# Optimization experiments

Hardware: AMD Instinct MI355X
Metric: run time of the kernel (lower is better)

The kernel has to match this reference:

```python
import jax, jax.numpy as jnp
import numpy as np
from jax import lax

B, S, F, C = 64, 2048, 256, 32


def setup_inputs() -> dict:
    key = jax.random.key(0)
    ks = jax.random.split(key, 6)
    return {
        "X": jax.random.normal(ks[0], (B, S, F), dtype=jnp.float32),
        "W": jax.random.normal(ks[1], (C, F), dtype=jnp.float32) * (1.0 / np.sqrt(F)),
        "b": jax.random.normal(ks[2], (C,), dtype=jnp.float32) * 0.01,
        "transitions": jax.random.normal(ks[3], (C, C), dtype=jnp.float32) * 0.1,
        "start_transitions": jax.random.normal(ks[4], (C,), dtype=jnp.float32) * 0.1,
        "end_transitions": jax.random.normal(ks[5], (C,), dtype=jnp.float32) * 0.1,
    }


def reference(X, W, b, transitions, start_transitions, end_transitions):
    # Affine projection to emission scores: [B, S, C]
    emissions = jnp.einsum("bsf,cf->bsc", X, W) + b
    e = jnp.moveaxis(emissions, 1, 0)  # [S, B, C] for scan over time

    alpha0 = start_transitions[None, :] + e[0]  # [B, C]

    def viterbi_step(alpha, e_t):
        # scores[b, i, j] = alpha[b, i] + T[i, j] + e_t[b, j]
        scores = alpha[:, :, None] + transitions[None, :, :] + e_t[:, None, :]
        best = jnp.max(scores, axis=1)      # [B, C]
        bp = jnp.argmax(scores, axis=1)     # [B, C] backpointers
        return best, bp

    alpha_T, backptrs = lax.scan(viterbi_step, alpha0, e[1:])  # backptrs: [S-1, B, C]

    final = alpha_T + end_transitions[None, :]
    best_score = jnp.max(final, axis=-1)              # [B]
    last_tag = jnp.argmax(final, axis=-1)             # [B]

    def backtrack(tag, bp):
        prev = jnp.take_along_axis(bp, tag[:, None], axis=1)[:, 0]
        return prev, prev

    _, prev_tags = lax.scan(backtrack, last_tag, backptrs, reverse=True)  # [S-1, B]
    path = jnp.concatenate([prev_tags, last_tag[None, :]], axis=0)        # [S, B]
    return best_score, jnp.moveaxis(path, 0, 1)  # ([B], [B, S])
```

## Files before the change

kernel.cpp:

```cpp
#include <hip/hip_runtime.h>

#define BB 64
#define SS 2048
#define FF 256
#define CC 32

typedef unsigned u32x2 __attribute__((ext_vector_type(2)));

__device__ __forceinline__ void plswap16(int a_in, int& x, int& y) {
#if __has_builtin(__builtin_amdgcn_permlane16_swap)
    u32x2 r = __builtin_amdgcn_permlane16_swap((unsigned)a_in, (unsigned)a_in, false, false);
    x = (int)r[0]; y = (int)r[1];
#else
    int xx = a_in, yy;
    asm volatile("v_mov_b32 %0, %1" : "=v"(yy) : "v"(a_in));
    asm volatile("v_permlane16_swap_b32 %0, %1" : "+v"(xx), "+v"(yy));
    x = xx; y = yy;
#endif
}
__device__ __forceinline__ void plswap32(int a_in, int& x, int& y) {
#if __has_builtin(__builtin_amdgcn_permlane32_swap)
    u32x2 r = __builtin_amdgcn_permlane32_swap((unsigned)a_in, (unsigned)a_in, false, false);
    x = (int)r[0]; y = (int)r[1];
#else
    int xx = a_in, yy;
    asm volatile("v_mov_b32 %0, %1" : "=v"(yy) : "v"(a_in));
    asm volatile("v_permlane32_swap_b32 %0, %1" : "+v"(xx), "+v"(yy));
    x = xx; y = yy;
#endif
}

#if __has_builtin(__builtin_amdgcn_mov_dpp)
#define ROT1(d, s, K) d = __builtin_amdgcn_mov_dpp(s, 0x120 + K, 0xF, 0xF, false)
#else
#define ROT1(d, s, K) d = __builtin_amdgcn_update_dpp(s, s, 0x120 + K, 0xF, 0xF, false)
#endif
#define ROTALL(arr, s) \
    arr[0] = s;        \
    ROT1(arr[1], s, 1);  ROT1(arr[2], s, 2);  ROT1(arr[3], s, 3);  \
    ROT1(arr[4], s, 4);  ROT1(arr[5], s, 5);  ROT1(arr[6], s, 6);  \
    ROT1(arr[7], s, 7);  ROT1(arr[8], s, 8);  ROT1(arr[9], s, 9);  \
    ROT1(arr[10], s, 10); ROT1(arr[11], s, 11); ROT1(arr[12], s, 12); \
    ROT1(arr[13], s, 13); ROT1(arr[14], s, 14); ROT1(arr[15], s, 15)

__device__ __forceinline__ float fmax3_(float a, float b, float c) { return fmaxf(fmaxf(a, b), c); }

__global__ __launch_bounds__(256) void emis_kernel(const float* __restrict__ X,
                                                   const float* __restrict__ W,
                                                   const float* __restrict__ bias,
                                                   float* __restrict__ em) {
    __shared__ __align__(16) float xs[64 * 260];
    __shared__ __align__(16) float wsh[32 * 260];
    const int tid = threadIdx.x;
    const long rowbase = (long)blockIdx.x * 64;

    const float4* Xg = (const float4*)(X + rowbase * FF);
#pragma unroll
    for (int i = 0; i < 16; ++i) {
        int idx = tid + i * 256;
        int r = idx >> 6, c4 = idx & 63;
        *(float4*)&xs[r * 260 + c4 * 4] = Xg[idx];
    }
    const float4* Wg = (const float4*)W;
#pragma unroll
    for (int i = 0; i < 8; ++i) {
        int idx = tid + i * 256;
        int r = idx >> 6, c4 = idx & 63;
        *(float4*)&wsh[r * 260 + c4 * 4] = Wg[idx];
    }
    __syncthreads();

    const int rp = tid >> 3;
    const int cg = (tid & 7) * 4;
    const int r0 = rp * 2, r1 = rp * 2 + 1;
    float acc0[4] = {0.f, 0.f, 0.f, 0.f};
    float acc1[4] = {0.f, 0.f, 0.f, 0.f};

#pragma unroll 4
    for (int k = 0; k < 256; k += 4) {
        float4 xa = *(const float4*)&xs[r0 * 260 + k];
        float4 xb = *(const float4*)&xs[r1 * 260 + k];
#pragma unroll
        for (int jj = 0; jj < 4; ++jj) {
            float4 w = *(const float4*)&wsh[(cg + jj) * 260 + k];
            acc0[jj] = fmaf(xa.x, w.x, acc0[jj]);
            acc0[jj] = fmaf(xa.y, w.y, acc0[jj]);
            acc0[jj] = fmaf(xa.z, w.z, acc0[jj]);
            acc0[jj] = fmaf(xa.w, w.w, acc0[jj]);
            acc1[jj] = fmaf(xb.x, w.x, acc1[jj]);
            acc1[jj] = fmaf(xb.y, w.y, acc1[jj]);
            acc1[jj] = fmaf(xb.z, w.z, acc1[jj]);
            acc1[jj] = fmaf(xb.w, w.w, acc1[jj]);
        }
    }
#pragma unroll
    for (int jj = 0; jj < 4; ++jj) {
        float bj = bias[cg + jj];
        em[(rowbase + r0) * CC + cg + jj] = acc0[jj] + bj;
        em[(rowbase + r1) * CC + cg + jj] = acc1[jj] + bj;
    }
}

#define STEP_ASM(avar, evar)                                                        \
    do {                                                                            \
        float x_, y_, b_, q0_, q1_, q2_, q3_, q4_, q5_, q6_, q7_,                   \
              q8_, q9_, q10_, q11_, q12_, q13_, q14_, q15_;                         \
        asm volatile(                                                               \
            "v_mov_b32 %[x], %[aa]\n\t"                                             \
            "s_nop 1\n\t"                                                           \
            "v_permlane16_swap_b32 %[x], %[aa]\n\t"                                 \
            "s_nop 0\n\t"                                                           \
            "v_cndmask_b32 %[bb], %[aa], %[x], %[m16]\n\t"                          \
            "s_nop 1\n\t"                                                           \
            "v_add_f32 %[q0], %[bb], %[t0]\n\t"                                     \
            "v_add_f32_dpp %[q1], %[bb], %[t1] row_ror:1 row_mask:0xf bank_mask:0xf\n\t"  \
            "v_add_f32_dpp %[q2], %[bb], %[t2] row_ror:2 row_mask:0xf bank_mask:0xf\n\t"  \
            "v_add_f32_dpp %[q3], %[bb], %[t3] row_ror:3 row_mask:0xf bank_mask:0xf\n\t"  \
            "v_add_f32_dpp %[q4], %[bb], %[t4] row_ror:4 row_mask:0xf bank_mask:0xf\n\t"  \
            "v_add_f32_dpp %[q5], %[bb], %[t5] row_ror:5 row_mask:0xf bank_mask:0xf\n\t"  \
            "v_add_f32_dpp %[q6], %[bb], %[t6] row_ror:6 row_mask:0xf bank_mask:0xf\n\t"  \
            "v_add_f32_dpp %[q7], %[bb], %[t7] row_ror:7 row_mask:0xf bank_mask:0xf\n\t"  \
            "v_add_f32_dpp %[q8], %[bb], %[t8] row_ror:8 row_mask:0xf bank_mask:0xf\n\t"  \
            "v_add_f32_dpp %[q9], %[bb], %[t9] row_ror:9 row_mask:0xf bank_mask:0xf\n\t"  \
            "v_add_f32_dpp %[q10], %[bb], %[t10] row_ror:10 row_mask:0xf bank_mask:0xf\n\t" \
            "v_add_f32_dpp %[q11], %[bb], %[t11] row_ror:11 row_mask:0xf bank_mask:0xf\n\t" \
            "v_add_f32_dpp %[q12], %[bb], %[t12] row_ror:12 row_mask:0xf bank_mask:0xf\n\t" \
            "v_add_f32_dpp %[q13], %[bb], %[t13] row_ror:13 row_mask:0xf bank_mask:0xf\n\t" \
            "v_add_f32_dpp %[q14], %[bb], %[t14] row_ror:14 row_mask:0xf bank_mask:0xf\n\t" \
            "v_add_f32_dpp %[q15], %[bb], %[t15] row_ror:15 row_mask:0xf bank_mask:0xf\n\t" \
            "v_max3_f32 %[q0], %[q0], %[q1], %[q2]\n\t"                             \
            "v_max3_f32 %[q3], %[q3], %[q4], %[q5]\n\t"                             \
            "v_max3_f32 %[q6], %[q6], %[q7], %[q8]\n\t"                             \
            "v_max3_f32 %[q9], %[q9], %[q10], %[q11]\n\t"                           \
            "v_max3_f32 %[q12], %[q12], %[q13], %[q14]\n\t"                         \
            "v_max3_f32 %[q0], %[q0], %[q3], %[q6]\n\t"                             \
            "v_max3_f32 %[q9], %[q9], %[q12], %[q15]\n\t"                           \
            "v_max_f32 %[q0], %[q0], %[q9]\n\t"                                     \
            "v_mov_b32 %[x], %[q0]\n\t"                                             \
            "v_mov_b32 %[y], %[q0]\n\t"                                             \
            "s_nop 1\n\t"                                                           \
            "v_permlane32_swap_b32 %[x], %[y]\n\t"                                  \
            "s_nop 0\n\t"                                                           \
            "v_cndmask_b32 %[y], %[y], %[x], %[m32]\n\t"                            \
            "v_max_f32 %[q0], %[q0], %[y]\n\t"                                      \
            "v_add_f32 %[aa], %[q0], %[ee]\n\t"                                     \
            : [aa] "+v"(avar), [x] "=&v"(x_), [y] "=&v"(y_), [bb] "=&v"(b_),        \
              [q0] "=&v"(q0_), [q1] "=&v"(q1_), [q2] "=&v"(q2_), [q3] "=&v"(q3_),   \
              [q4] "=&v"(q4_), [q5] "=&v"(q5_), [q6] "=&v"(q6_), [q7] "=&v"(q7_),   \
              [q8] "=&v"(q8_), [q9] "=&v"(q9_), [q10] "=&v"(q10_),                  \
              [q11] "=&v"(q11_), [q12] "=&v"(q12_), [q13] "=&v"(q13_),              \
              [q14] "=&v"(q14_), [q15] "=&v"(q15_)                                  \
            : [ee] "v"(evar), [t0] "v"(Ti[0]), [t1] "v"(Ti[1]), [t2] "v"(Ti[2]),    \
              [t3] "v"(Ti[3]), [t4] "v"(Ti[4]), [t5] "v"(Ti[5]), [t6] "v"(Ti[6]),   \
              [t7] "v"(Ti[7]), [t8] "v"(Ti[8]), [t9] "v"(Ti[9]), [t10] "v"(Ti[10]), \
              [t11] "v"(Ti[11]), [t12] "v"(Ti[12]), [t13] "v"(Ti[13]),              \
              [t14] "v"(Ti[14]), [t15] "v"(Ti[15]),                                 \
              [m16] "s"(mask16), [m32] "s"(mask32));                                \
    } while (0)

__global__ __launch_bounds__(64, 1) void viterbi_fwd4(float* __restrict__ em,
                                                      const float* __restrict__ T,
                                                      const float* __restrict__ startT,
                                                      const float* __restrict__ endT,
                                                      float* __restrict__ out) {
    const int l = threadIdx.x;
    const int b = blockIdx.x;
    const int j = l & 31;
    const int h = l >> 5;

    int p0, p1;
    plswap16(j, p0, p1);
    const bool c16 = (((p0 >> 4) & 1) == h);
    const int pm = c16 ? p0 : p1;
    int mk[16];
    ROTALL(mk, pm);
    int q0, q1;
    plswap32(l, q0, q1);
    const bool pick0 = (q0 == (l ^ 32));

    const unsigned long long mask16 = __ballot(c16);
    const unsigned long long mask32 = __ballot(pick0);

    float Ti[16];
#pragma unroll
    for (int k = 0; k < 16; ++k) Ti[k] = T[mk[k] * CC + j];

    float* eb = em + (long)b * SS * CC;

    float eq[8];
#pragma unroll
    for (int v = 0; v < 8; ++v) eq[v] = eb[v * 32 + j];

    float a = startT[j] + eq[0];
    eb[j] = a;
    eq[0] = eb[8 * 32 + j];

    int t = 1;
    for (int g = 0; g < 254; ++g) {
#pragma unroll
        for (int u = 0; u < 8; ++u) {
            STEP_ASM(a, eq[t & 7]);
            eb[t * 32 + j] = a;
            eq[t & 7] = eb[(t + 8) * 32 + j];
            ++t;
        }
    }
#pragma unroll
    for (int u = 0; u < 7; ++u) {
        STEP_ASM(a, eq[t & 7]);
        eb[t * 32 + j] = a;
        eq[t & 7] = eb[(t + 8) * 32 + j];
        ++t;
    }
#pragma unroll
    for (int u = 0; u < 8; ++u) {
        STEP_ASM(a, eq[t & 7]);
        eb[t * 32 + j] = a;
        ++t;
    }

    float v = a + endT[j];
    int idx = j;
#pragma unroll
    for (int d = 1; d <= 16; d <<= 1) {
        float ovv = __shfl_xor(v, d);
        int   oii = __shfl_xor(idx, d);
        bool c = (ovv > v) || (ovv == v && oii < idx);
        v = c ? ovv : v;
        idx = c ? oii : idx;
    }
    if (l == 0) {
        out[b] = v;
        out[BB + (long)b * SS + (SS - 1)] = (float)idx;
    }
}

__global__ __launch_bounds__(64, 2) void bp_compose(const float* __restrict__ alpha,
                                                    const float* __restrict__ T,
                                                    unsigned* __restrict__ bp,
                                                    unsigned char* __restrict__ G) {
    const int l = threadIdx.x;
    const int j = l & 31;
    const int h = l >> 5;
    const int b = blockIdx.x >> 5;
    const int k = blockIdx.x & 31;

    int p0, p1;
    plswap16(j, p0, p1);
    const bool c16 = (((p0 >> 4) & 1) == h);
    const int pm = c16 ? p0 : p1;
    int mk[16];
    ROTALL(mk, pm);
    int q0, q1;
    plswap32(l, q0, q1);
    const bool pick0 = (q0 == (l ^ 32));

    float Ti[16];
    unsigned Bk[16];
#pragma unroll
    for (int kk = 0; kk < 16; ++kk) {
        Ti[kk] = T[mk[kk] * CC + j];
        Bk[kk] = 1u << mk[kk];
    }

    const float* A = alpha + (long)b * SS * CC;
    const int kk0 = k << 6;

    float aq[8];
#pragma unroll
    for (int v = 0; v < 8; ++v) aq[v] = A[(kk0 + v) * CC + j];

    unsigned sr[16];
#pragma unroll
    for (int p = 0; p < 16; ++p) sr[p] = 0u;

#pragma unroll
    for (int g8 = 0; g8 < 8; ++g8) {
#pragma unroll
        for (int v = 0; v < 8; ++v) {
            const int u = g8 * 8 + v;
            float av = aq[v];
            if (g8 < 7) aq[v] = A[(kk0 + (g8 + 1) * 8 + v) * CC + j];

            int x, y;
            plswap16(__float_as_int(av), x, y);
            int base = c16 ? x : y;
            int rot[16];
            ROTALL(rot, base);
            float s[16];
#pragma unroll
            for (int kk = 0; kk < 16; ++kk) s[kk] = __int_as_float(rot[kk]) + Ti[kk];

            float m0 = fmax3_(s[0], s[1], s[2]);
            float m1 = fmax3_(s[3], s[4], s[5]);
            float m2 = fmax3_(s[6], s[7], s[8]);
            float m3 = fmax3_(s[9], s[10], s[11]);
            float m4 = fmax3_(s[12], s[13], s[14]);
            float mv = fmaxf(fmax3_(m0, m1, m2), fmax3_(m3, m4, s[15]));

            int xm, ym;
            plswap32(__float_as_int(mv), xm, ym);
            float ov = __int_as_float(pick0 ? xm : ym);
            float gv = fmaxf(mv, ov);

            unsigned c0 = (s[0] == gv) ? Bk[0] : 0u,   c1 = (s[1] == gv) ? Bk[1] : 0u;
            unsigned c2 = (s[2] == gv) ? Bk[2] : 0u,   c3 = (s[3] == gv) ? Bk[3] : 0u;
            unsigned c4 = (s[4] == gv) ? Bk[4] : 0u,   c5 = (s[5] == gv) ? Bk[5] : 0u;
            unsigned c6 = (s[6] == gv) ? Bk[6] : 0u,   c7 = (s[7] == gv) ? Bk[7] : 0u;
            unsigned c8 = (s[8] == gv) ? Bk[8] : 0u,   c9 = (s[9] == gv) ? Bk[9] : 0u;
            unsigned c10 = (s[10] == gv) ? Bk[10] : 0u, c11 = (s[11] == gv) ? Bk[11] : 0u;
            unsigned c12 = (s[12] == gv) ? Bk[12] : 0u, c13 = (s[13] == gv) ? Bk[13] : 0u;
            unsigned c14 = (s[14] == gv) ? Bk[14] : 0u, c15 = (s[15] == gv) ? Bk[15] : 0u;
            unsigned msk = ((c0 | c1 | c2) | (c3 | c4 | c5)) |
                           ((c6 | c7 | c8) | (c9 | c10 | c11)) |
                           ((c12 | c13 | c14) | c15);

            int xk, yk;
            plswap32((int)msk, xk, yk);
            unsigned om = (unsigned)(pick0 ? xk : yk);
            int wi = __builtin_ctz(msk | om);

            if (u == 63) {
                if (kk0 + 63 == SS - 1) wi = j;
            }
            sr[u >> 2] |= (unsigned)wi << ((u & 3) * 8);
        }
    }

#pragma unroll
    for (int p = 0; p < 16; ++p)
        bp[((unsigned)(16 * k + p) * BB + b) * CC + j] = sr[p];

    int g = j;
#pragma unroll
    for (int rel = 63; rel >= 0; --rel) {
        unsigned dw = (unsigned)__builtin_amdgcn_ds_bpermute((g | (l & 32)) << 2,
                                                             (int)sr[rel >> 2]);
        g = (int)((dw >> ((rel & 3) * 8)) & 31u);
    }
    G[(b * 32 + k) * 32 + j] = (unsigned char)g;
}

__global__ __launch_bounds__(64) void bt_emit2(const unsigned* __restrict__ bp,
                                               const unsigned char* __restrict__ G,
                                               float* __restrict__ out) {
    const int l = threadIdx.x;
    const int b = blockIdx.x >> 5;
    const int k = blockIdx.x & 31;

    unsigned sr[16];
#pragma unroll
    for (int p = 0; p < 16; ++p) sr[p] = bp[((unsigned)(16 * k + p) * BB + b) * CC + (l & 31)];

    int cur = (int)out[BB + (long)b * SS + (SS - 1)];
    for (int kk = 31; kk > k; --kk) cur = (int)G[(b * 32 + kk) * 32 + cur];

    int g = cur, cap = cur;
#pragma unroll
    for (int rel = 63; rel >= 0; --rel) {
        unsigned dw = (unsigned)__builtin_amdgcn_ds_bpermute((g | (l & 32)) << 2,
                                                             (int)sr[rel >> 2]);
        g = (int)((dw >> ((rel & 3) * 8)) & 31u);
        cap = (l == rel) ? g : cap;
    }
    out[BB + (long)b * SS + k * 64 + l] = (float)cap;
}

extern "C" void kernel_launch(void* const* d_in, const int* in_sizes, int n_in,
                              void* d_out, int out_size, void* d_ws, size_t ws_size,
                              hipStream_t stream) {
    const float* X      = (const float*)d_in[0];
    const float* W      = (const float*)d_in[1];
    const float* bias   = (const float*)d_in[2];
    const float* T      = (const float*)d_in[3];
    const float* startT = (const float*)d_in[4];
    const float* endT   = (const float*)d_in[5];
    float* out = (float*)d_out;

    float*    em = (float*)d_ws;
    unsigned* bp = (unsigned*)((char*)d_ws + (size_t)BB * SS * CC * 4);
    unsigned char* G = (unsigned char*)d_ws + (20u << 20);

    emis_kernel<<<(BB * SS) / 64, 256, 0, stream>>>(X, W, bias, em);
    viterbi_fwd4<<<BB, 64, 0, stream>>>(em, T, startT, endT, out);
    bp_compose<<<BB * 32, 64, 0, stream>>>(em, T, bp, G);
    bt_emit2<<<BB * 32, 64, 0, stream>>>(bp, G, out);
}
```

Baseline: 307.9 us.

## Fuse forward recursion with backpointer compose via LDS ring and flag sync

The forward max-plus recursion now runs on one wave per batch row and writes alpha into an 8-slot shared-memory ring. Three helper waves in the same block poll a progress flag and compute backpointers and 64-step chunk compositions concurrently, so the separate bp_compose kernel and the global alpha round trip go away. The suffix composition over chunks moves into a single-block bt_scan kernel, replacing the per-block quadratic G walk in the emit kernel. The step also drops a mask-select after the permlane32 swap. The risks are a ring-overrun race if the consumer waves fall behind, spin-wait overhead, and only one block per batch row.

Measured after the change: 323.8 us. 1.05x slower.

```diff
diff --git a/kernel.cpp b/kernel.cpp
--- a/kernel.cpp
+++ b/kernel.cpp
@@ -101,9 +101,9 @@
     }
 }
 
-#define STEP_ASM(avar, evar)                                                        \
+#define STEP2_ASM(avar, evar)                                                       \
     do {                                                                            \
-        float x_, y_, b_, q0_, q1_, q2_, q3_, q4_, q5_, q6_, q7_,                   \
+        float x_, b_, q0_, q1_, q2_, q3_, q4_, q5_, q6_, q7_,                       \
               q8_, q9_, q10_, q11_, q12_, q13_, q14_, q15_;                         \
         asm volatile(                                                               \
             "v_mov_b32 %[x], %[aa]\n\t"                                             \
@@ -137,14 +137,12 @@
             "v_max3_f32 %[q9], %[q9], %[q12], %[q15]\n\t"                           \
             "v_max_f32 %[q0], %[q0], %[q9]\n\t"                                     \
             "v_mov_b32 %[x], %[q0]\n\t"                                             \
-            "v_mov_b32 %[y], %[q0]\n\t"                                             \
             "s_nop 1\n\t"                                                           \
-            "v_permlane32_swap_b32 %[x], %[y]\n\t"                                  \
+            "v_permlane32_swap_b32 %[x], %[q0]\n\t"                                 \
             "s_nop 0\n\t"                                                           \
-            "v_cndmask_b32 %[y], %[y], %[x], %[m32]\n\t"                            \
-            "v_max_f32 %[q0], %[q0], %[y]\n\t"                                      \
+            "v_max_f32 %[q0], %[q0], %[x]\n\t"                                      \
             "v_add_f32 %[aa], %[q0], %[ee]\n\t"                                     \
-            : [aa] "+v"(avar), [x] "=&v"(x_), [y] "=&v"(y_), [bb] "=&v"(b_),        \
+            : [aa] "+v"(avar), [x] "=&v"(x_), [bb] "=&v"(b_),                       \
               [q0] "=&v"(q0_), [q1] "=&v"(q1_), [q2] "=&v"(q2_), [q3] "=&v"(q3_),   \
               [q4] "=&v"(q4_), [q5] "=&v"(q5_), [q6] "=&v"(q6_), [q7] "=&v"(q7_),   \
               [q8] "=&v"(q8_), [q9] "=&v"(q9_), [q10] "=&v"(q10_),                  \
@@ -155,18 +153,28 @@
               [t7] "v"(Ti[7]), [t8] "v"(Ti[8]), [t9] "v"(Ti[9]), [t10] "v"(Ti[10]), \
               [t11] "v"(Ti[11]), [t12] "v"(Ti[12]), [t13] "v"(Ti[13]),              \
               [t14] "v"(Ti[14]), [t15] "v"(Ti[15]),                                 \
-              [m16] "s"(mask16), [m32] "s"(mask32));                                \
+              [m16] "s"(mask16));                                                   \
     } while (0)
 
-__global__ __launch_bounds__(64, 1) void viterbi_fwd4(float* __restrict__ em,
-                                                      const float* __restrict__ T,
-                                                      const float* __restrict__ startT,
-                                                      const float* __restrict__ endT,
-                                                      float* __restrict__ out) {
-    const int l = threadIdx.x;
+__global__ __launch_bounds__(256, 1) void viterbi_fused(const float* __restrict__ em,
+                                                        const float* __restrict__ T,
+                                                        const float* __restrict__ startT,
+                                                        const float* __restrict__ endT,
+                                                        unsigned* __restrict__ bp,
+                                                        unsigned char* __restrict__ G,
+                                                        float* __restrict__ out) {
+    __shared__ float aring[8 * 2048];
+    __shared__ int prog;
+
+    const int tid = threadIdx.x;
+    const int w = tid >> 6;
+    const int l = tid & 63;
     const int b = blockIdx.x;
     const int j = l & 31;
     const int h = l >> 5;
+
+    if (tid == 0) prog = 0;
+    __syncthreads();
 
     int p0, p1;
     plswap16(j, p0, p1);
@@ -174,176 +182,204 @@
     const int pm = c16 ? p0 : p1;
     int mk[16];
     ROTALL(mk, pm);
-    int q0, q1;
-    plswap32(l, q0, q1);
-    const bool pick0 = (q0 == (l ^ 32));
-
-    const unsigned long long mask16 = __ballot(c16);
-    const unsigned long long mask32 = __ballot(pick0);
+    int q0p, q1p;
+    plswap32(l, q0p, q1p);
+    const bool pick0 = (q0p == (l ^ 32));
 
     float Ti[16];
 #pragma unroll
     for (int k = 0; k < 16; ++k) Ti[k] = T[mk[k] * CC + j];
 
-    float* eb = em + (long)b * SS * CC;
-
-    float eq[8];
-#pragma unroll
-    for (int v = 0; v < 8; ++v) eq[v] = eb[v * 32 + j];
-
-    float a = startT[j] + eq[0];
-    eb[j] = a;
-    eq[0] = eb[8 * 32 + j];
-
-    int t = 1;
-    for (int g = 0; g < 254; ++g) {
-#pragma unroll
-        for (int u = 0; u < 8; ++u) {
-            STEP_ASM(a, eq[t & 7]);
-            eb[t * 32 + j] = a;
-            eq[t & 7] = eb[(t + 8) * 32 + j];
-            ++t;
-        }
-    }
-#pragma unroll
-    for (int u = 0; u < 7; ++u) {
-        STEP_ASM(a, eq[t & 7]);
-        eb[t * 32 + j] = a;
-        eq[t & 7] = eb[(t + 8) * 32 + j];
-        ++t;
-    }
-#pragma unroll
-    for (int u = 0; u < 8; ++u) {
-        STEP_ASM(a, eq[t & 7]);
-        eb[t * 32 + j] = a;
-        ++t;
-    }
-
-    float v = a + endT[j];
-    int idx = j;
-#pragma unroll
-    for (int d = 1; d <= 16; d <<= 1) {
-        float ovv = __shfl_xor(v, d);
-        int   oii = __shfl_xor(idx, d);
-        bool c = (ovv > v) || (ovv == v && oii < idx);
-        v = c ? ovv : v;
-        idx = c ? oii : idx;
-    }
-    if (l == 0) {
-        out[b] = v;
-        out[BB + (long)b * SS + (SS - 1)] = (float)idx;
-    }
-}
-
-__global__ __launch_bounds__(64, 2) void bp_compose(const float* __restrict__ alpha,
-                                                    const float* __restrict__ T,
-                                                    unsigned* __restrict__ bp,
-                                                    unsigned char* __restrict__ G) {
+    if (w == 0) {
+        const unsigned long long mask16 = __ballot(c16);
+        const float* eb = em + (long)b * SS * CC;
+
+        float eq[8];
+#pragma unroll
+        for (int v = 0; v < 8; ++v) eq[v] = eb[v * 32 + j];
+
+        float a = startT[j] + eq[0];
+        aring[j] = a;
+        eq[0] = eb[8 * 32 + j];
+
+        auto flagset = [&](int v) {
+            asm volatile("s_waitcnt lgkmcnt(0)" ::: "memory");
+            if (l == 0) *(volatile int*)&prog = v;
+        };
+
+#pragma unroll
+        for (int uu = 1; uu < 8; ++uu) {
+            STEP2_ASM(a, eq[uu]);
+            aring[uu * 32 + j] = a;
+            eq[uu] = eb[(uu + 8) * 32 + j];
+        }
+        for (int u8 = 1; u8 < 8; ++u8) {
+#pragma unroll
+            for (int uu = 0; uu < 8; ++uu) {
+                int u = u8 * 8 + uu;
+                STEP2_ASM(a, eq[uu]);
+                aring[u * 32 + j] = a;
+                eq[uu] = eb[(u + 8) * 32 + j];
+            }
+        }
+        flagset(1);
+
+        for (int c = 1; c < 31; ++c) {
+            const int tb = c << 6;
+            float* slot = &aring[(c & 7) * 2048];
+            for (int u8 = 0; u8 < 8; ++u8) {
+#pragma unroll
+                for (int uu = 0; uu < 8; ++uu) {
+                    int u = u8 * 8 + uu;
+                    STEP2_ASM(a, eq[uu]);
+                    slot[u * 32 + j] = a;
+                    eq[uu] = eb[(tb + u + 8) * 32 + j];
+                }
+            }
+            flagset(c + 1);
+        }
+
+        {
+            float* slot = &aring[(31 & 7) * 2048];
+            for (int u8 = 0; u8 < 7; ++u8) {
+#pragma unroll
+                for (int uu = 0; uu < 8; ++uu) {
+                    int u = u8 * 8 + uu;
+                    STEP2_ASM(a, eq[uu]);
+                    slot[u * 32 + j] = a;
+                    eq[uu] = eb[(1984 + u + 8) * 32 + j];
+                }
+            }
+#pragma unroll
+            for (int uu = 0; uu < 8; ++uu) {
+                int u = 56 + uu;
+                STEP2_ASM(a, eq[uu]);
+                slot[u * 32 + j] = a;
+            }
+            flagset(32);
+        }
+
+        float v = a + endT[j];
+        int idx = j;
+#pragma unroll
+        for (int d = 1; d <= 16; d <<= 1) {
+            float ovv = __shfl_xor(v, d);
+            int   oii = __shfl_xor(idx, d);
+            bool c = (ovv > v) || (ovv == v && oii < idx);
+            v = c ? ovv : v;
+            idx = c ? oii : idx;
+        }
+        if (l == 0) {
+            out[b] = v;
+            out[BB + (long)b * SS + (SS - 1)] = (float)idx;
+        }
+    } else {
+        unsigned Bk[16];
+#pragma unroll
+        for (int kk = 0; kk < 16; ++kk) Bk[kk] = 1u << mk[kk];
+
+        for (int c = w - 1; c < 32; c += 3) {
+            while (*(volatile int*)&prog < c + 1) __builtin_amdgcn_s_sleep(2);
+            asm volatile("" ::: "memory");
+            const float* AS = &aring[(c & 7) * 2048];
+
+            float aq[8];
+#pragma unroll
+            for (int v = 0; v < 8; ++v) aq[v] = AS[v * 32 + j];
+
+            unsigned sr[16];
+#pragma unroll
+            for (int p = 0; p < 16; ++p) sr[p] = 0u;
+
+#pragma unroll
+            for (int g8 = 0; g8 < 8; ++g8) {
+#pragma unroll
+                for (int v = 0; v < 8; ++v) {
+                    const int u = g8 * 8 + v;
+                    float av = aq[v];
+                    if (g8 < 7) aq[v] = AS[((g8 + 1) * 8 + v) * 32 + j];
+
+                    int x, y;
+                    plswap16(__float_as_int(av), x, y);
+                    int base = c16 ? x : y;
+                    int rot[16];
+                    ROTALL(rot, base);
+                    float s[16];
+#pragma unroll
+                    for (int kk = 0; kk < 16; ++kk) s[kk] = __int_as_float(rot[kk]) + Ti[kk];
+
+                    float m0 = fmax3_(s[0], s[1], s[2]);
+                    float m1 = fmax3_(s[3], s[4], s[5]);
+                    float m2 = fmax3_(s[6], s[7], s[8]);
+                    float m3 = fmax3_(s[9], s[10], s[11]);
+                    float m4 = fmax3_(s[12], s[13], s[14]);
+                    float mv = fmaxf(fmax3_(m0, m1, m2), fmax3_(m3, m4, s[15]));
+
+                    int xm, ym;
+                    plswap32(__float_as_int(mv), xm, ym);
+                    float ov = __int_as_float(pick0 ? xm : ym);
+                    float gv = fmaxf(mv, ov);
+
+                    unsigned c0 = (s[0] == gv) ? Bk[0] : 0u,   c1 = (s[1] == gv) ? Bk[1] : 0u;
+                    unsigned c2 = (s[2] == gv) ? Bk[2] : 0u,   c3 = (s[3] == gv) ? Bk[3] : 0u;
+                    unsigned c4 = (s[4] == gv) ? Bk[4] : 0u,   c5 = (s[5] == gv) ? Bk[5] : 0u;
+                    unsigned c6 = (s[6] == gv) ? Bk[6] : 0u,   c7 = (s[7] == gv) ? Bk[7] : 0u;
+                    unsigned c8 = (s[8] == gv) ? Bk[8] : 0u,   c9 = (s[9] == gv) ? Bk[9] : 0u;
+                    unsigned c10 = (s[10] == gv) ? Bk[10] : 0u, c11 = (s[11] == gv) ? Bk[11] : 0u;
+                    unsigned c12 = (s[12] == gv) ? Bk[12] : 0u, c13 = (s[13] == gv) ? Bk[13] : 0u;
+                    unsigned c14 = (s[14] == gv) ? Bk[14] : 0u, c15 = (s[15] == gv) ? Bk[15] : 0u;
+                    unsigned msk = ((c0 | c1 | c2) | (c3 | c4 | c5)) |
+                                   ((c6 | c7 | c8) | (c9 | c10 | c11)) |
+                                   ((c12 | c13 | c14) | c15);
+
+                    int xk, yk;
+                    plswap32((int)msk, xk, yk);
+                    unsigned om = (unsigned)(pick0 ? xk : yk);
+                    int wi = __builtin_ctz(msk | om);
+
+                    if (u == 63 && c == 31) wi = j;
+                    sr[u >> 2] |= (unsigned)wi << ((u & 3) * 8);
+                }
+            }
+
+#pragma unroll
+            for (int p = 0; p < 16; ++p)
+                bp[((unsigned)(16 * c + p) * BB + b) * CC + j] = sr[p];
+
+            int g = j;
+#pragma unroll
+            for (int rel = 63; rel >= 0; --rel) {
+                unsigned dw = (unsigned)__builtin_amdgcn_ds_bpermute((g | (l & 32)) << 2,
+                                                                     (int)sr[rel >> 2]);
+                g = (int)((dw >> ((rel & 3) * 8)) & 31u);
+            }
+            G[(b * 32 + c) * 32 + j] = (unsigned char)g;
+        }
+    }
+}
+
+__global__ __launch_bounds__(64) void bt_scan(const unsigned char* __restrict__ G,
+                                              const float* __restrict__ out,
+                                              int* __restrict__ tagB) {
+    __shared__ unsigned char Gs[64 * 32 * 32];
     const int l = threadIdx.x;
-    const int j = l & 31;
-    const int h = l >> 5;
-    const int b = blockIdx.x >> 5;
-    const int k = blockIdx.x & 31;
-
-    int p0, p1;
-    plswap16(j, p0, p1);
-    const bool c16 = (((p0 >> 4) & 1) == h);
-    const int pm = c16 ? p0 : p1;
-    int mk[16];
-    ROTALL(mk, pm);
-    int q0, q1;
-    plswap32(l, q0, q1);
-    const bool pick0 = (q0 == (l ^ 32));
-
-    float Ti[16];
-    unsigned Bk[16];
-#pragma unroll
-    for (int kk = 0; kk < 16; ++kk) {
-        Ti[kk] = T[mk[kk] * CC + j];
-        Bk[kk] = 1u << mk[kk];
-    }
-
-    const float* A = alpha + (long)b * SS * CC;
-    const int kk0 = k << 6;
-
-    float aq[8];
-#pragma unroll
-    for (int v = 0; v < 8; ++v) aq[v] = A[(kk0 + v) * CC + j];
-
-    unsigned sr[16];
-#pragma unroll
-    for (int p = 0; p < 16; ++p) sr[p] = 0u;
-
-#pragma unroll
-    for (int g8 = 0; g8 < 8; ++g8) {
-#pragma unroll
-        for (int v = 0; v < 8; ++v) {
-            const int u = g8 * 8 + v;
-            float av = aq[v];
-            if (g8 < 7) aq[v] = A[(kk0 + (g8 + 1) * 8 + v) * CC + j];
-
-            int x, y;
-            plswap16(__float_as_int(av), x, y);
-            int base = c16 ? x : y;
-            int rot[16];
-            ROTALL(rot, base);
-            float s[16];
-#pragma unroll
-            for (int kk = 0; kk < 16; ++kk) s[kk] = __int_as_float(rot[kk]) + Ti[kk];
-
-            float m0 = fmax3_(s[0], s[1], s[2]);
-            float m1 = fmax3_(s[3], s[4], s[5]);
-            float m2 = fmax3_(s[6], s[7], s[8]);
-            float m3 = fmax3_(s[9], s[10], s[11]);
-            float m4 = fmax3_(s[12], s[13], s[14]);
-            float mv = fmaxf(fmax3_(m0, m1, m2), fmax3_(m3, m4, s[15]));
-
-            int xm, ym;
-            plswap32(__float_as_int(mv), xm, ym);
-            float ov = __int_as_float(pick0 ? xm : ym);
-            float gv = fmaxf(mv, ov);
-
-            unsigned c0 = (s[0] == gv) ? Bk[0] : 0u,   c1 = (s[1] == gv) ? Bk[1] : 0u;
-            unsigned c2 = (s[2] == gv) ? Bk[2] : 0u,   c3 = (s[3] == gv) ? Bk[3] : 0u;
-            unsigned c4 = (s[4] == gv) ? Bk[4] : 0u,   c5 = (s[5] == gv) ? Bk[5] : 0u;
-            unsigned c6 = (s[6] == gv) ? Bk[6] : 0u,   c7 = (s[7] == gv) ? Bk[7] : 0u;
-            unsigned c8 = (s[8] == gv) ? Bk[8] : 0u,   c9 = (s[9] == gv) ? Bk[9] : 0u;
-            unsigned c10 = (s[10] == gv) ? Bk[10] : 0u, c11 = (s[11] == gv) ? Bk[11] : 0u;
-            unsigned c12 = (s[12] == gv) ? Bk[12] : 0u, c13 = (s[13] == gv) ? Bk[13] : 0u;
-            unsigned c14 = (s[14] == gv) ? Bk[14] : 0u, c15 = (s[15] == gv) ? Bk[15] : 0u;
-            unsigned msk = ((c0 | c1 | c2) | (c3 | c4 | c5)) |
-                           ((c6 | c7 | c8) | (c9 | c10 | c11)) |
-                           ((c12 | c13 | c14) | c15);
-
-            int xk, yk;
-            plswap32((int)msk, xk, yk);
-            unsigned om = (unsigned)(pick0 ? xk : yk);
-            int wi = __builtin_ctz(msk | om);
-
-            if (u == 63) {
-                if (kk0 + 63 == SS - 1) wi = j;
-            }
-            sr[u >> 2] |= (unsigned)wi << ((u & 3) * 8);
-        }
-    }
-
-#pragma unroll
-    for (int p = 0; p < 16; ++p)
-        bp[((unsigned)(16 * k + p) * BB + b) * CC + j] = sr[p];
-
-    int g = j;
-#pragma unroll
-    for (int rel = 63; rel >= 0; --rel) {
-        unsigned dw = (unsigned)__builtin_amdgcn_ds_bpermute((g | (l & 32)) << 2,
-                                                             (int)sr[rel >> 2]);
-        g = (int)((dw >> ((rel & 3) * 8)) & 31u);
-    }
-    G[(b * 32 + k) * 32 + j] = (unsigned char)g;
-}
-
-__global__ __launch_bounds__(64) void bt_emit2(const unsigned* __restrict__ bp,
-                                               const unsigned char* __restrict__ G,
-                                               float* __restrict__ out) {
+    const float4* Gg = (const float4*)G;
+    float4* Gls = (float4*)Gs;
+#pragma unroll
+    for (int i = 0; i < 64; ++i) Gls[l + i * 64] = Gg[l + i * 64];
+    __syncthreads();
+
+    const int b = l;
+    int cur = (int)out[BB + (long)b * SS + (SS - 1)];
+    for (int k = 31; k >= 0; --k) {
+        cur = Gs[(b * 32 + k) * 32 + cur];
+        tagB[b * 32 + k] = cur;
+    }
+}
+
+__global__ __launch_bounds__(64) void bt_emit(const unsigned* __restrict__ bp,
+                                              const int* __restrict__ tagB,
+                                              float* __restrict__ out) {
     const int l = threadIdx.x;
     const int b = blockIdx.x >> 5;
     const int k = blockIdx.x & 31;
@@ -352,10 +388,9 @@
 #pragma unroll
     for (int p = 0; p < 16; ++p) sr[p] = bp[((unsigned)(16 * k + p) * BB + b) * CC + (l & 31)];
 
-    int cur = (int)out[BB + (long)b * SS + (SS - 1)];
-    for (int kk = 31; kk > k; --kk) cur = (int)G[(b * 32 + kk) * 32 + cur];
-
-    int g = cur, cap = cur;
+    int start = (k == 31) ? (int)out[BB + (long)b * SS + (SS - 1)]
+                          : tagB[b * 32 + k + 1];
+    int g = start, cap = start;
 #pragma unroll
     for (int rel = 63; rel >= 0; --rel) {
         unsigned dw = (unsigned)__builtin_amdgcn_ds_bpermute((g | (l & 32)) << 2,
@@ -379,10 +414,11 @@
 
     float*    em = (float*)d_ws;
     unsigned* bp = (unsigned*)((char*)d_ws + (size_t)BB * SS * CC * 4);
-    unsigned char* G = (unsigned char*)d_ws + (20u << 20);
+    unsigned char* G    = (unsigned char*)d_ws + (20u << 20);
+    int*           tagB = (int*)((char*)d_ws + (20u << 20) + 65536);
 
     emis_kernel<<<(BB * SS) / 64, 256, 0, stream>>>(X, W, bias, em);
-    viterbi_fwd4<<<BB, 64, 0, stream>>>(em, T, startT, endT, out);
-    bp_compose<<<BB * 32, 64, 0, stream>>>(em, T, bp, G);
-    bt_emit2<<<BB * 32, 64, 0, stream>>>(bp, G, out);
-}
+    viterbi_fused<<<BB, 256, 0, stream>>>(em, T, startT, endT, bp, G, out);
+    bt_scan<<<1, 64, 0, stream>>>(G, out, tagB);
+    bt_emit<<<BB * 32, 64, 0, stream>>>(bp, tagB, out);
+}
```

## Split backtrack into smaller chunks with separate serial scan of chunk maps

Applied to the files above, without the earlier changes.

Halves the backtrack chunk length to 32 steps, giving 64 chunks per sequence, and doubles bp_compose's occupancy hint. A new tiny bt_scan kernel does the serial composition of chunk maps once per batch from shared memory, so each emit block no longer walks all later chunk maps itself. The forward step drops a cndmask and extra mov by using the permlane32_swap result directly. The emission store is vectorised to float4. This adds one extra launch and a serial kernel running on only two blocks.

Measured after the change: 291.1 us. -5.5%, faster.

```diff
diff --git a/kernel.cpp b/kernel.cpp
--- a/kernel.cpp
+++ b/kernel.cpp
@@ -4,6 +4,7 @@
 #define SS 2048
 #define FF 256
 #define CC 32
+#define CH 64
 
 typedef unsigned u32x2 __attribute__((ext_vector_type(2)));
 
@@ -93,17 +94,16 @@
             acc1[jj] = fmaf(xb.w, w.w, acc1[jj]);
         }
     }
-#pragma unroll
-    for (int jj = 0; jj < 4; ++jj) {
-        float bj = bias[cg + jj];
-        em[(rowbase + r0) * CC + cg + jj] = acc0[jj] + bj;
-        em[(rowbase + r1) * CC + cg + jj] = acc1[jj] + bj;
-    }
-}
-
-#define STEP_ASM(avar, evar)                                                        \
+    float4 b4 = *(const float4*)&bias[cg];
+    float4 o0 = make_float4(acc0[0] + b4.x, acc0[1] + b4.y, acc0[2] + b4.z, acc0[3] + b4.w);
+    float4 o1 = make_float4(acc1[0] + b4.x, acc1[1] + b4.y, acc1[2] + b4.z, acc1[3] + b4.w);
+    *(float4*)&em[(rowbase + r0) * CC + cg] = o0;
+    *(float4*)&em[(rowbase + r1) * CC + cg] = o1;
+}
+
+#define STEP2_ASM(avar, evar)                                                       \
     do {                                                                            \
-        float x_, y_, b_, q0_, q1_, q2_, q3_, q4_, q5_, q6_, q7_,                   \
+        float x_, b_, q0_, q1_, q2_, q3_, q4_, q5_, q6_, q7_,                       \
               q8_, q9_, q10_, q11_, q12_, q13_, q14_, q15_;                         \
         asm volatile(                                                               \
             "v_mov_b32 %[x], %[aa]\n\t"                                             \
@@ -137,14 +137,12 @@
             "v_max3_f32 %[q9], %[q9], %[q12], %[q15]\n\t"                           \
             "v_max_f32 %[q0], %[q0], %[q9]\n\t"                                     \
             "v_mov_b32 %[x], %[q0]\n\t"                                             \
-            "v_mov_b32 %[y], %[q0]\n\t"                                             \
             "s_nop 1\n\t"                                                           \
-            "v_permlane32_swap_b32 %[x], %[y]\n\t"                                  \
+            "v_permlane32_swap_b32 %[x], %[q0]\n\t"                                 \
             "s_nop 0\n\t"                                                           \
-            "v_cndmask_b32 %[y], %[y], %[x], %[m32]\n\t"                            \
-            "v_max_f32 %[q0], %[q0], %[y]\n\t"                                      \
+            "v_max_f32 %[q0], %[q0], %[x]\n\t"                                      \
             "v_add_f32 %[aa], %[q0], %[ee]\n\t"                                     \
-            : [aa] "+v"(avar), [x] "=&v"(x_), [y] "=&v"(y_), [bb] "=&v"(b_),        \
+            : [aa] "+v"(avar), [x] "=&v"(x_), [bb] "=&v"(b_),                       \
               [q0] "=&v"(q0_), [q1] "=&v"(q1_), [q2] "=&v"(q2_), [q3] "=&v"(q3_),   \
               [q4] "=&v"(q4_), [q5] "=&v"(q5_), [q6] "=&v"(q6_), [q7] "=&v"(q7_),   \
               [q8] "=&v"(q8_), [q9] "=&v"(q9_), [q10] "=&v"(q10_),                  \
@@ -155,7 +153,7 @@
               [t7] "v"(Ti[7]), [t8] "v"(Ti[8]), [t9] "v"(Ti[9]), [t10] "v"(Ti[10]), \
               [t11] "v"(Ti[11]), [t12] "v"(Ti[12]), [t13] "v"(Ti[13]),              \
               [t14] "v"(Ti[14]), [t15] "v"(Ti[15]),                                 \
-              [m16] "s"(mask16), [m32] "s"(mask32));                                \
+              [m16] "s"(mask16));                                                   \
     } while (0)
 
 __global__ __launch_bounds__(64, 1) void viterbi_fwd4(float* __restrict__ em,
@@ -174,12 +172,8 @@
     const int pm = c16 ? p0 : p1;
     int mk[16];
     ROTALL(mk, pm);
-    int q0, q1;
-    plswap32(l, q0, q1);
-    const bool pick0 = (q0 == (l ^ 32));
 
     const unsigned long long mask16 = __ballot(c16);
-    const unsigned long long mask32 = __ballot(pick0);
 
     float Ti[16];
 #pragma unroll
@@ -199,7 +193,7 @@
     for (int g = 0; g < 254; ++g) {
 #pragma unroll
         for (int u = 0; u < 8; ++u) {
-            STEP_ASM(a, eq[t & 7]);
+            STEP2_ASM(a, eq[t & 7]);
             eb[t * 32 + j] = a;
             eq[t & 7] = eb[(t + 8) * 32 + j];
             ++t;
@@ -207,14 +201,14 @@
     }
 #pragma unroll
     for (int u = 0; u < 7; ++u) {
-        STEP_ASM(a, eq[t & 7]);
+        STEP2_ASM(a, eq[t & 7]);
         eb[t * 32 + j] = a;
         eq[t & 7] = eb[(t + 8) * 32 + j];
         ++t;
     }
 #pragma unroll
     for (int u = 0; u < 8; ++u) {
-        STEP_ASM(a, eq[t & 7]);
+        STEP2_ASM(a, eq[t & 7]);
         eb[t * 32 + j] = a;
         ++t;
     }
@@ -235,15 +229,15 @@
     }
 }
 
-__global__ __launch_bounds__(64, 2) void bp_compose(const float* __restrict__ alpha,
+__global__ __launch_bounds__(64, 4) void bp_compose(const float* __restrict__ alpha,
                                                     const float* __restrict__ T,
                                                     unsigned* __restrict__ bp,
                                                     unsigned char* __restrict__ G) {
     const int l = threadIdx.x;
     const int j = l & 31;
     const int h = l >> 5;
-    const int b = blockIdx.x >> 5;
-    const int k = blockIdx.x & 31;
+    const int b = blockIdx.x >> 6;
+    const int k = blockIdx.x & 63;
 
     int p0, p1;
     plswap16(j, p0, p1);
@@ -251,9 +245,9 @@
     const int pm = c16 ? p0 : p1;
     int mk[16];
     ROTALL(mk, pm);
-    int q0, q1;
-    plswap32(l, q0, q1);
-    const bool pick0 = (q0 == (l ^ 32));
+    int q0p, q1p;
+    plswap32(l, q0p, q1p);
+    const bool pick0 = (q0p == (l ^ 32));
 
     float Ti[16];
     unsigned Bk[16];
@@ -264,23 +258,23 @@
     }
 
     const float* A = alpha + (long)b * SS * CC;
-    const int kk0 = k << 6;
+    const int u0 = k << 5;
 
     float aq[8];
 #pragma unroll
-    for (int v = 0; v < 8; ++v) aq[v] = A[(kk0 + v) * CC + j];
-
-    unsigned sr[16];
-#pragma unroll
-    for (int p = 0; p < 16; ++p) sr[p] = 0u;
-
-#pragma unroll
-    for (int g8 = 0; g8 < 8; ++g8) {
+    for (int v = 0; v < 8; ++v) aq[v] = A[(u0 + v) * CC + j];
+
+    unsigned sr[8];
+#pragma unroll
+    for (int p = 0; p < 8; ++p) sr[p] = 0u;
+
+#pragma unroll
+    for (int g8 = 0; g8 < 4; ++g8) {
 #pragma unroll
         for (int v = 0; v < 8; ++v) {
             const int u = g8 * 8 + v;
             float av = aq[v];
-            if (g8 < 7) aq[v] = A[(kk0 + (g8 + 1) * 8 + v) * CC + j];
+            if (g8 < 3) aq[v] = A[(u0 + (g8 + 1) * 8 + v) * CC + j];
 
             int x, y;
             plswap16(__float_as_int(av), x, y);
@@ -320,50 +314,70 @@
             unsigned om = (unsigned)(pick0 ? xk : yk);
             int wi = __builtin_ctz(msk | om);
 
-            if (u == 63) {
-                if (kk0 + 63 == SS - 1) wi = j;
-            }
+            if (u == 31 && k == CH - 1) wi = j;
             sr[u >> 2] |= (unsigned)wi << ((u & 3) * 8);
         }
     }
 
 #pragma unroll
-    for (int p = 0; p < 16; ++p)
-        bp[((unsigned)(16 * k + p) * BB + b) * CC + j] = sr[p];
+    for (int p = 0; p < 8; ++p)
+        bp[((unsigned)(8 * k + p) * BB + b) * CC + j] = sr[p];
 
     int g = j;
 #pragma unroll
-    for (int rel = 63; rel >= 0; --rel) {
+    for (int rel = 31; rel >= 0; --rel) {
         unsigned dw = (unsigned)__builtin_amdgcn_ds_bpermute((g | (l & 32)) << 2,
                                                              (int)sr[rel >> 2]);
         g = (int)((dw >> ((rel & 3) * 8)) & 31u);
     }
-    G[(b * 32 + k) * 32 + j] = (unsigned char)g;
-}
-
-__global__ __launch_bounds__(64) void bt_emit2(const unsigned* __restrict__ bp,
-                                               const unsigned char* __restrict__ G,
-                                               float* __restrict__ out) {
+    G[(b * CH + k) * 32 + j] = (unsigned char)g;
+}
+
+__global__ __launch_bounds__(64) void bt_scan(const unsigned char* __restrict__ G,
+                                              const float* __restrict__ out,
+                                              int* __restrict__ tagB) {
+    __shared__ unsigned char Gs[32 * CH * 32];
     const int l = threadIdx.x;
-    const int b = blockIdx.x >> 5;
-    const int k = blockIdx.x & 31;
-
-    unsigned sr[16];
-#pragma unroll
-    for (int p = 0; p < 16; ++p) sr[p] = bp[((unsigned)(16 * k + p) * BB + b) * CC + (l & 31)];
-
-    int cur = (int)out[BB + (long)b * SS + (SS - 1)];
-    for (int kk = 31; kk > k; --kk) cur = (int)G[(b * 32 + kk) * 32 + cur];
-
-    int g = cur, cap = cur;
-#pragma unroll
-    for (int rel = 63; rel >= 0; --rel) {
+    const int bbase = blockIdx.x * 32;
+    const float4* Gg = (const float4*)(G + (size_t)bbase * CH * 32);
+    float4* Gls = (float4*)Gs;
+#pragma unroll
+    for (int i = 0; i < 64; ++i) Gls[l + i * 64] = Gg[l + i * 64];
+    __syncthreads();
+
+    if (l < 32) {
+        const int b = bbase + l;
+        int cur = (int)out[BB + (long)b * SS + (SS - 1)];
+        for (int k = CH - 1; k >= 0; --k) {
+            cur = Gs[(l * CH + k) * 32 + cur];
+            tagB[b * CH + k] = cur;
+        }
+    }
+}
+
+__global__ __launch_bounds__(64, 4) void bt_emit(const unsigned* __restrict__ bp,
+                                                 const int* __restrict__ tagB,
+                                                 const float* __restrict__ outR,
+                                                 float* __restrict__ out) {
+    const int l = threadIdx.x;
+    const int b = blockIdx.x >> 6;
+    const int k = blockIdx.x & 63;
+
+    unsigned sr[8];
+#pragma unroll
+    for (int p = 0; p < 8; ++p) sr[p] = bp[((unsigned)(8 * k + p) * BB + b) * CC + (l & 31)];
+
+    int start = (k == CH - 1) ? (int)outR[BB + (long)b * SS + (SS - 1)]
+                              : tagB[b * CH + k + 1];
+    int g = start, cap = start;
+#pragma unroll
+    for (int rel = 31; rel >= 0; --rel) {
         unsigned dw = (unsigned)__builtin_amdgcn_ds_bpermute((g | (l & 32)) << 2,
                                                              (int)sr[rel >> 2]);
         g = (int)((dw >> ((rel & 3) * 8)) & 31u);
         cap = (l == rel) ? g : cap;
     }
-    out[BB + (long)b * SS + k * 64 + l] = (float)cap;
+    if (l < 32) out[BB + (long)b * SS + k * 32 + l] = (float)cap;
 }
 
 extern "C" void kernel_launch(void* const* d_in, const int* in_sizes, int n_in,
@@ -379,10 +393,12 @@
 
     float*    em = (float*)d_ws;
     unsigned* bp = (unsigned*)((char*)d_ws + (size_t)BB * SS * CC * 4);
-    unsigned char* G = (unsigned char*)d_ws + (20u << 20);
+    unsigned char* G    = (unsigned char*)d_ws + (20u << 20);
+    int*           tagB = (int*)((char*)d_ws + (20u << 20) + 131072);
 
     emis_kernel<<<(BB * SS) / 64, 256, 0, stream>>>(X, W, bias, em);
     viterbi_fwd4<<<BB, 64, 0, stream>>>(em, T, startT, endT, out);
-    bp_compose<<<BB * 32, 64, 0, stream>>>(em, T, bp, G);
-    bt_emit2<<<BB * 32, 64, 0, stream>>>(bp, G, out);
-}
+    bp_compose<<<BB * CH, 64, 0, stream>>>(em, T, bp, G);
+    bt_scan<<<2, 64, 0, stream>>>(G, out, tagB);
+    bt_emit<<<BB * CH, 64, 0, stream>>>(bp, tagB, out, out);
+}
```
